# Kernel optimization log

Measured on AMD Instinct MI355X. Metric: run time of the kernel, lower is better.

The kernel has to match this reference:

```python
import jax, jax.numpy as jnp
import numpy as np

N, E, C, H0, H1 = 100_000, 1_600_000, 32, 128, 64


def _sage(x, src, dst, wl, bl, wr, n):
    # PyG SAGEConv(aggr='min'): lin_l(min_{j in N(i)} x_j) + lin_r(x_i); lin_r has no bias.
    agg = jax.ops.segment_min(x[src], dst, num_segments=n)  # [n, d]
    # nodes with no in-edges: PyG fills with 0 (segment_min yields dtype max)
    agg = jnp.where(agg >= jnp.finfo(x.dtype).max, jnp.zeros((), x.dtype), agg)
    return agg @ wl + bl + x @ wr


def _bn(x, g, b, eps=1e-5):
    # training-mode BatchNorm over the node dimension
    mu = jnp.mean(x, axis=0)
    var = jnp.var(x, axis=0)
    return (x - mu) * jax.lax.rsqrt(var + eps) * g + b


def _forward(x, edge_index,
             rm1_wl, rm1_bl, rm1_wr, rmn1_g, rmn1_b,
             rm2_wl, rm2_bl, rm2_wr, rmn2_g, rmn2_b,
             rm4_wl, rm4_bl, rm4_wr,
             sh1_wl, sh1_bl, sh1_wr, shn1_g, shn1_b,
             rt1_wl, rt1_bl, rt1_wr, rtn1_g, rtn1_b, rt3_w, rt3_b,
             md1_wl, md1_bl, md1_wr, mdn1_g, mdn1_b, md3_w, md3_b):
    n = x.shape[0]
    src, dst = edge_index[0], edge_index[1]
    rm = jax.nn.relu(_bn(_sage(x, src, dst, rm1_wl, rm1_bl, rm1_wr, n), rmn1_g, rmn1_b))
    rm = jax.nn.relu(_bn(_sage(rm, src, dst, rm2_wl, rm2_bl, rm2_wr, n), rmn2_g, rmn2_b))
    rm = _sage(rm, src, dst, rm4_wl, rm4_bl, rm4_wr, n)  # [n, 3]
    xs = jnp.concatenate([x, rm], axis=1)  # [n, C+3]
    xs = jax.nn.relu(_bn(_sage(xs, src, dst, sh1_wl, sh1_bl, sh1_wr, n), shn1_g, shn1_b))
    rm_ls = jax.nn.log_softmax(rm, axis=1)
    labels = (jnp.argmax(rm_ls, axis=1) == 2).astype(x.dtype)  # [n]
    rt = jax.nn.relu(_bn(_sage(xs, src, dst, rt1_wl, rt1_bl, rt1_wr, n), rtn1_g, rtn1_b))
    rt = (rt @ rt3_w + rt3_b).ravel() * labels
    md = jax.nn.relu(_bn(_sage(xs, src, dst, md1_wl, md1_bl, md1_wr, n), mdn1_g, mdn1_b))
    md = (md @ md3_w + md3_b).ravel() * labels
    return rm_ls, rt, md


def setup_inputs() -> dict:
    key = jax.random.key(0)
    ks = iter(jax.random.split(key, 64))

    def w(shape):
        s = 1.0 / np.sqrt(shape[0])
        return jax.random.uniform(next(ks), shape, jnp.float32, -s, s)

    inp = {
        "x": jax.random.normal(next(ks), (N, C), jnp.float32),
        "edge_index": jax.random.randint(next(ks), (2, E), 0, N, dtype=jnp.int32),
    }

    def sage_params(cin, cout, name):
        inp[name + "_wl"] = w((cin, cout))
        inp[name + "_bl"] = jnp.zeros((cout,), jnp.float32)
        inp[name + "_wr"] = w((cin, cout))

    def bn_params(c, name):
        inp[name + "_g"] = jnp.ones((c,), jnp.float32)
        inp[name + "_b"] = jnp.zeros((c,), jnp.float32)

    sage_params(C, H0, "rm1"); bn_params(H0, "rmn1")
    sage_params(H0, H1, "rm2"); bn_params(H1, "rmn2")
    sage_params(H1, 3, "rm4")
    sage_params(C + 3, H0, "sh1"); bn_params(H0, "shn1")
    sage_params(H0, H1, "rt1"); bn_params(H1, "rtn1")
    inp["rt3_w"] = w((H1, 1)); inp["rt3_b"] = jnp.zeros((1,), jnp.float32)
    sage_params(H0, H1, "md1"); bn_params(H1, "mdn1")
    inp["md3_w"] = w((H1, 1)); inp["md3_b"] = jnp.zeros((1,), jnp.float32)
    return inp


def reference(x, edge_index,
              rm1_wl, rm1_bl, rm1_wr, rmn1_g, rmn1_b,
              rm2_wl, rm2_bl, rm2_wr, rmn2_g, rmn2_b,
              rm4_wl, rm4_bl, rm4_wr,
              sh1_wl, sh1_bl, sh1_wr, shn1_g, shn1_b,
              rt1_wl, rt1_bl, rt1_wr, rtn1_g, rtn1_b, rt3_w, rt3_b,
              md1_wl, md1_bl, md1_wr, mdn1_g, mdn1_b, md3_w, md3_b):
    return _forward(x, edge_index,
                    rm1_wl, rm1_bl, rm1_wr, rmn1_g, rmn1_b,
                    rm2_wl, rm2_bl, rm2_wr, rmn2_g, rmn2_b,
                    rm4_wl, rm4_bl, rm4_wr,
                    sh1_wl, sh1_bl, sh1_wr, shn1_g, shn1_b,
                    rt1_wl, rt1_bl, rt1_wr, rtn1_g, rtn1_b, rt3_w, rt3_b,
                    md1_wl, md1_bl, md1_wr, mdn1_g, mdn1_b, md3_w, md3_b)
```

## Files before the change

kernel.cpp:

```cpp
#include <hip/hip_runtime.h>

#define FLTMAX 3.402823466e+38f
#define DEV __device__ __forceinline__

typedef unsigned short u16;
typedef unsigned int u32;
typedef __bf16 bf16_t;
typedef bf16_t bf16x8 __attribute__((ext_vector_type(8)));
typedef float f32x4 __attribute__((ext_vector_type(4)));

union U16x8 { uint4 u; bf16x8 b; };

DEV float trf(float v, float a, float b) { return fmaxf(fmaf(v, a, b), 0.f); }

DEV float sfmin(float m, float v, u32 sm) {
    return fminf(m, __uint_as_float(__float_as_uint(v) ^ sm));
}
DEV float sdec(float m, u32 sm) { return __uint_as_float(__float_as_uint(m) ^ sm); }

DEV u16 f2bf(float f) {
    u32 u = __float_as_uint(f);
    return (u16)((u + 0x7FFFu + ((u >> 16) & 1u)) >> 16);
}

__global__ __launch_bounds__(256) void hist_k(const int* __restrict__ dst,
                                              int* __restrict__ deg, int E) {
    int e = blockIdx.x * 256 + threadIdx.x;
    if (e >= E) return;
    atomicAdd(&deg[dst[e]], 1);
}

__global__ __launch_bounds__(256) void scan_block_k(const int* __restrict__ deg,
                                                    int* __restrict__ ptr,
                                                    int* __restrict__ bsum, int n) {
    __shared__ int ls[256];
    int i = blockIdx.x * 256 + threadIdx.x;
    int v = (i < n) ? deg[i] : 0;
    ls[threadIdx.x] = v;
    __syncthreads();
#pragma unroll
    for (int off = 1; off < 256; off <<= 1) {
        int a = (threadIdx.x >= off) ? ls[threadIdx.x - off] : 0;
        __syncthreads();
        ls[threadIdx.x] += a;
        __syncthreads();
    }
    if (i < n) ptr[i] = ls[threadIdx.x] - v;
    if (threadIdx.x == 255) bsum[blockIdx.x] = ls[255];
}

__global__ __launch_bounds__(512) void scan_bsum_k(int* __restrict__ bsum, int nb) {
    __shared__ int ls[512];
    int t = threadIdx.x;
    int v = (t < nb) ? bsum[t] : 0;
    ls[t] = v;
    __syncthreads();
#pragma unroll
    for (int off = 1; off < 512; off <<= 1) {
        int a = (t >= off) ? ls[t - off] : 0;
        __syncthreads();
        ls[t] += a;
        __syncthreads();
    }
    if (t < nb) bsum[t] = ls[t] - v;
}

__global__ __launch_bounds__(256) void scan_add_k(int* __restrict__ ptr,
                                                  int* __restrict__ pos,
                                                  const int* __restrict__ bsum,
                                                  int n, int E) {
    int i = blockIdx.x * 256 + threadIdx.x;
    if (i == 0) ptr[n] = E;
    if (i < n) {
        int p = ptr[i] + bsum[blockIdx.x];
        ptr[i] = p;
        pos[i] = p;
    }
}

__global__ __launch_bounds__(256) void csr_fill_part_k(
    const int* __restrict__ src, const int* __restrict__ dst,
    int* __restrict__ pos, int* __restrict__ csr, int E, int lo_step) {
    const int part = blockIdx.x & 7;
    const int e = (blockIdx.x >> 3) * 256 + threadIdx.x;
    if (e >= E) return;
    const int d = dst[e];
    const int lo = part * lo_step;
    const int hi = lo + lo_step;
    if (d < lo || d >= hi) return;
    const int p = atomicAdd(&pos[d], 1);
    csr[p] = src[e];
}

__global__ __launch_bounds__(256) void gather_min32_k(
    const float* __restrict__ feat, const int* __restrict__ ptr,
    const int* __restrict__ csr, float* __restrict__ agg, int n) {
    const int lane = threadIdx.x & 63;
    const int wave = (blockIdx.x * 256 + threadIdx.x) >> 6;
    const int node = wave * 2 + (lane >> 5);
    if (node >= n) return;
    const int fl = lane & 31;
    int e = ptr[node];
    const int end = ptr[node + 1];
    const bool empty = (e == end);
    float m = FLTMAX;
    for (; e + 7 < end; e += 8) {
        int s[8];
#pragma unroll
        for (int j = 0; j < 8; j++) s[j] = csr[e + j];
        float v[8];
#pragma unroll
        for (int j = 0; j < 8; j++) v[j] = feat[(size_t)s[j] * 32 + fl];
#pragma unroll
        for (int j = 0; j < 8; j++) m = fminf(m, v[j]);
    }
    for (; e < end; e++) m = fminf(m, feat[(size_t)csr[e] * 32 + fl]);
    agg[(size_t)node * 32 + fl] = empty ? 0.f : m;
}

__global__ __launch_bounds__(256) void gather_min128_k(
    const float* __restrict__ feat, const int* __restrict__ ptr,
    const int* __restrict__ csr, const float* __restrict__ coef,
    float* __restrict__ agg, int n) {
    const int lane = threadIdx.x & 63;
    const int wave = (blockIdx.x * 256 + threadIdx.x) >> 6;
    const int node = wave * 2 + (lane >> 5);
    if (node >= n) return;
    const int fl = (lane & 31) * 4;
    const float4 ca = *(const float4*)(coef + fl);
    const float4 cb = *(const float4*)(coef + 128 + fl);
    const u32 sm0 = (ca.x < 0.f) ? 0x80000000u : 0u;
    const u32 sm1 = (ca.y < 0.f) ? 0x80000000u : 0u;
    const u32 sm2 = (ca.z < 0.f) ? 0x80000000u : 0u;
    const u32 sm3 = (ca.w < 0.f) ? 0x80000000u : 0u;
    int e = ptr[node];
    const int end = ptr[node + 1];
    const bool empty = (e == end);
    float m0 = FLTMAX, m1 = FLTMAX, m2 = FLTMAX, m3 = FLTMAX;
    for (; e + 7 < end; e += 8) {
        int s[8];
#pragma unroll
        for (int j = 0; j < 8; j++) s[j] = csr[e + j];
        float4 v[8];
#pragma unroll
        for (int j = 0; j < 8; j++) v[j] = *(const float4*)(feat + (size_t)s[j] * 128 + fl);
#pragma unroll
        for (int j = 0; j < 8; j++) {
            m0 = sfmin(m0, v[j].x, sm0);
            m1 = sfmin(m1, v[j].y, sm1);
            m2 = sfmin(m2, v[j].z, sm2);
            m3 = sfmin(m3, v[j].w, sm3);
        }
    }
    for (; e + 3 < end; e += 4) {
        int s[4];
#pragma unroll
        for (int j = 0; j < 4; j++) s[j] = csr[e + j];
        float4 v[4];
#pragma unroll
        for (int j = 0; j < 4; j++) v[j] = *(const float4*)(feat + (size_t)s[j] * 128 + fl);
#pragma unroll
        for (int j = 0; j < 4; j++) {
            m0 = sfmin(m0, v[j].x, sm0);
            m1 = sfmin(m1, v[j].y, sm1);
            m2 = sfmin(m2, v[j].z, sm2);
            m3 = sfmin(m3, v[j].w, sm3);
        }
    }
    for (; e < end; e++) {
        const float4 v = *(const float4*)(feat + (size_t)csr[e] * 128 + fl);
        m0 = sfmin(m0, v.x, sm0);
        m1 = sfmin(m1, v.y, sm1);
        m2 = sfmin(m2, v.z, sm2);
        m3 = sfmin(m3, v.w, sm3);
    }
    float4 o;
    o.x = empty ? 0.f : trf(sdec(m0, sm0), ca.x, cb.x);
    o.y = empty ? 0.f : trf(sdec(m1, sm1), ca.y, cb.y);
    o.z = empty ? 0.f : trf(sdec(m2, sm2), ca.z, cb.z);
    o.w = empty ? 0.f : trf(sdec(m3, sm3), ca.w, cb.w);
    *(float4*)(agg + (size_t)node * 128 + fl) = o;
}

__global__ __launch_bounds__(256) void gather_bf_k(
    u16* __restrict__ Acat, const int* __restrict__ ptr,
    const int* __restrict__ csr, int n) {
    const int lane = threadIdx.x & 63;
    const int wave = (blockIdx.x * 256 + threadIdx.x) >> 6;
    const int node = wave * 2 + (lane >> 5);
    if (node >= n) return;
    const int fl = (lane & 31) * 4;
    int e = ptr[node];
    const int end = ptr[node + 1];
    uint2 outv = {0u, 0u};
    if (e != end) {
        float m0 = FLTMAX, m1 = FLTMAX, m2 = FLTMAX, m3 = FLTMAX;
        for (; e + 7 < end; e += 8) {
            int s[8];
#pragma unroll
            for (int j = 0; j < 8; j++) s[j] = csr[e + j];
            uint2 v[8];
#pragma unroll
            for (int j = 0; j < 8; j++) v[j] = *(const uint2*)(Acat + (size_t)s[j] * 256 + 128 + fl);
#pragma unroll
            for (int j = 0; j < 8; j++) {
                m0 = fminf(m0, __uint_as_float(v[j].x << 16));
                m1 = fminf(m1, __uint_as_float(v[j].x & 0xffff0000u));
                m2 = fminf(m2, __uint_as_float(v[j].y << 16));
                m3 = fminf(m3, __uint_as_float(v[j].y & 0xffff0000u));
            }
        }
        for (; e < end; e++) {
            const uint2 v = *(const uint2*)(Acat + (size_t)csr[e] * 256 + 128 + fl);
            m0 = fminf(m0, __uint_as_float(v.x << 16));
            m1 = fminf(m1, __uint_as_float(v.x & 0xffff0000u));
            m2 = fminf(m2, __uint_as_float(v.y << 16));
            m3 = fminf(m3, __uint_as_float(v.y & 0xffff0000u));
        }
        outv.x = (__float_as_uint(m0) >> 16) | (__float_as_uint(m1) & 0xffff0000u);
        outv.y = (__float_as_uint(m2) >> 16) | (__float_as_uint(m3) & 0xffff0000u);
    }
    *(uint2*)(Acat + (size_t)node * 256 + fl) = outv;
}

__global__ __launch_bounds__(256) void gather_min3_k(
    const float* __restrict__ feat, const int* __restrict__ ptr,
    const int* __restrict__ csr, float* __restrict__ agg, int n) {
    int i = blockIdx.x * 256 + threadIdx.x;
    if (i >= n) return;
    int e = ptr[i], end = ptr[i + 1];
    bool empty = (e == end);
    float m0 = FLTMAX, m1 = FLTMAX, m2 = FLTMAX;
    for (; e < end; e++) {
        const float* r = feat + (size_t)csr[e] * 3;
        m0 = fminf(m0, r[0]);
        m1 = fminf(m1, r[1]);
        m2 = fminf(m2, r[2]);
    }
    agg[(size_t)i * 3 + 0] = empty ? 0.f : m0;
    agg[(size_t)i * 3 + 1] = empty ? 0.f : m1;
    agg[(size_t)i * 3 + 2] = empty ? 0.f : m2;
}

__global__ __launch_bounds__(256) void convert_k(
    const float* __restrict__ h, const float* __restrict__ coef,
    u16* __restrict__ Acat, int n) {
    int t = blockIdx.x * 256 + threadIdx.x;
    int total = n * 32;
    if (t >= total) return;
    int i = t >> 5;
    int dq = (t & 31) * 4;
    const float4 hv = *(const float4*)(h + (size_t)i * 128 + dq);
    const float4 ca = *(const float4*)(coef + dq);
    const float4 cb = *(const float4*)(coef + 128 + dq);
    ushort4 o;
    o.x = f2bf(trf(hv.x, ca.x, cb.x));
    o.y = f2bf(trf(hv.y, ca.y, cb.y));
    o.z = f2bf(trf(hv.z, ca.z, cb.z));
    o.w = f2bf(trf(hv.w, ca.w, cb.w));
    *(ushort4*)(Acat + (size_t)i * 256 + 128 + dq) = o;
}

__global__ __launch_bounds__(256) void wprep_dual_k(
    const float* __restrict__ rwl, const float* __restrict__ rwr,
    const float* __restrict__ mwl, const float* __restrict__ mwr,
    u16* __restrict__ WT) {
    int t = blockIdx.x * 256 + threadIdx.x;
    int c = t >> 8;
    int k = t & 255;
    const float* wlp = (c < 64) ? rwl : mwl;
    const float* wrp = (c < 64) ? rwr : mwr;
    const int cc = c & 63;
    float v = (k < 128) ? wlp[k * 64 + cc] : wrp[(k - 128) * 64 + cc];
    WT[(size_t)c * 256 + k] = f2bf(v);
}

__global__ __launch_bounds__(256) void gemm_bf_k(
    const u16* __restrict__ A, const u16* __restrict__ WT,
    const float* __restrict__ bl1, const float* __restrict__ bl2,
    float* __restrict__ out, float* __restrict__ bpart, int n) {
    constexpr int NT = 8;
    __shared__ float bs[256];
    const int tid = threadIdx.x;
    bs[tid] = 0.f;
    const int wave = tid >> 6, lane = tid & 63;
    const int quad = lane >> 4, l16 = lane & 15;
    const int row0 = blockIdx.x * 64 + wave * 16;
    const int rowA = min(row0 + l16, n - 1);
    const uint4* Arow = (const uint4*)(A + (size_t)rowA * 256) + quad;

    bf16x8 a[8];
#pragma unroll
    for (int kc = 0; kc < 8; kc++) {
        U16x8 u; u.u = Arow[kc * 4];
        a[kc] = u.b;
    }
    f32x4 acc[NT];
#pragma unroll
    for (int i = 0; i < NT; i++) acc[i] = (f32x4){0.f, 0.f, 0.f, 0.f};
#pragma unroll
    for (int nt = 0; nt < NT; nt++) {
        const uint4* Brow = (const uint4*)(WT + (size_t)(nt * 16 + l16) * 256) + quad;
#pragma unroll
        for (int kc = 0; kc < 8; kc++) {
            U16x8 u; u.u = Brow[kc * 4];
            acc[nt] = __builtin_amdgcn_mfma_f32_16x16x32_bf16(a[kc], u.b, acc[nt], 0, 0, 0);
        }
    }
    __syncthreads();
#pragma unroll
    for (int nt = 0; nt < NT; nt++) {
        const int col = nt * 16 + l16;
        const float bias = (col < 64) ? bl1[col] : bl2[col - 64];
        float s = 0.f, q = 0.f;
#pragma unroll
        for (int r = 0; r < 4; r++) {
            const int row = row0 + quad * 4 + r;
            if (row < n) {
                const float o = acc[nt][r] + bias;
                out[(size_t)row * 128 + col] = o;
                s += o;
                q += o * o;
            }
        }
        atomicAdd(&bs[col], s);
        atomicAdd(&bs[128 + col], q);
    }
    __syncthreads();
    bpart[(size_t)blockIdx.x * 256 + tid] = bs[tid];
}

__global__ __launch_bounds__(256) void linear1s_k(
    const float* __restrict__ agg, const float* __restrict__ h,
    const float* __restrict__ wl, const float* __restrict__ bl,
    const float* __restrict__ wr, float* __restrict__ out,
    float* __restrict__ bpart, int n) {
    constexpr int DOUT = 128, CT = 32, RB = 32, LDW = 36;
    __shared__ float Ash[RB * LDW];
    __shared__ float Hsh[RB * LDW];
    const int tid = threadIdx.x;
    const int base = blockIdx.x * RB;
    {
        const int sr = tid >> 3;
        const int col = (tid & 7) * 4;
        const int grow = min(base + sr, n - 1);
        *(float4*)(Ash + sr * LDW + col) = *(const float4*)(agg + (size_t)grow * 32 + col);
        *(float4*)(Hsh + sr * LDW + col) = *(const float4*)(h + (size_t)grow * 32 + col);
    }
    __syncthreads();
    const int ct = tid % CT;
    const int rt = tid / CT;
    const int col = ct * 4;
    const int row0 = base + rt * 4;
    float4 acc[4] = {};
#pragma unroll 2
    for (int k0 = 0; k0 < 32; k0 += 4) {
        float4 wlv[4], wrv[4];
#pragma unroll
        for (int j = 0; j < 4; j++) {
            wlv[j] = *(const float4*)(wl + (size_t)(k0 + j) * DOUT + col);
            wrv[j] = *(const float4*)(wr + (size_t)(k0 + j) * DOUT + col);
        }
#pragma unroll
        for (int r = 0; r < 4; r++) {
            const float4 av = *(const float4*)(Ash + (rt * 4 + r) * LDW + k0);
            const float4 hv = *(const float4*)(Hsh + (rt * 4 + r) * LDW + k0);
#pragma unroll
            for (int j = 0; j < 4; j++) {
                const float aa = j == 0 ? av.x : j == 1 ? av.y : j == 2 ? av.z : av.w;
                const float bb = j == 0 ? hv.x : j == 1 ? hv.y : j == 2 ? hv.z : hv.w;
                acc[r].x += aa * wlv[j].x + bb * wrv[j].x;
                acc[r].y += aa * wlv[j].y + bb * wrv[j].y;
                acc[r].z += aa * wlv[j].z + bb * wrv[j].z;
                acc[r].w += aa * wlv[j].w + bb * wrv[j].w;
            }
        }
    }
    const float4 bv = *(const float4*)(bl + col);
    float cs[4] = {}, cq[4] = {};
#pragma unroll
    for (int r = 0; r < 4; r++) {
        if (row0 + r < n) {
            float4 o = acc[r];
            o.x += bv.x; o.y += bv.y; o.z += bv.z; o.w += bv.w;
            *(float4*)(out + (size_t)(row0 + r) * DOUT + col) = o;
            cs[0] += o.x; cq[0] += o.x * o.x;
            cs[1] += o.y; cq[1] += o.y * o.y;
            cs[2] += o.z; cq[2] += o.z * o.z;
            cs[3] += o.w; cq[3] += o.w * o.w;
        }
    }
    __syncthreads();
#pragma unroll
    for (int j = 0; j < 4; j++) Ash[tid * 4 + j] = cs[j];
    __syncthreads();
    if (tid < CT) {
#pragma unroll
        for (int j = 0; j < 4; j++) {
            float s = 0.f;
#pragma unroll
            for (int k = 0; k < 8; k++) s += Ash[(tid + k * CT) * 4 + j];
            bpart[(size_t)blockIdx.x * 256 + tid * 4 + j] = s;
        }
    }
    __syncthreads();
#pragma unroll
    for (int j = 0; j < 4; j++) Ash[tid * 4 + j] = cq[j];
    __syncthreads();
    if (tid < CT) {
#pragma unroll
        for (int j = 0; j < 4; j++) {
            float s = 0.f;
#pragma unroll
            for (int k = 0; k < 8; k++) s += Ash[(tid + k * CT) * 4 + j];
            bpart[(size_t)blockIdx.x * 256 + 128 + tid * 4 + j] = s;
        }
    }
}

__global__ __launch_bounds__(256) void linear2_k(
    const float* __restrict__ agg, const float* __restrict__ h,
    const float* __restrict__ coef, const float* __restrict__ wl,
    const float* __restrict__ bl, const float* __restrict__ wr,
    float* __restrict__ out, float* __restrict__ bpart, int n) {
    constexpr int DIN = 128, DOUT = 64, CT = 16, RB = 64, LDW = 132;
    __shared__ float Ash[RB * LDW];
    __shared__ float Hsh[RB * LDW];
    const int tid = threadIdx.x;
    const int base = blockIdx.x * RB;
    {
        const int sr = tid >> 2;
        const int sc = tid & 3;
        const int grow = min(base + sr, n - 1);
        const float* ar = agg + (size_t)grow * DIN;
        const float* hr = h + (size_t)grow * DIN;
#pragma unroll
        for (int c = 0; c < 8; c++) {
            const int col = (sc + c * 4) * 4;
            const float4 av = *(const float4*)(ar + col);
            float4 hv = *(const float4*)(hr + col);
            const float4 ca = *(const float4*)(coef + col);
            const float4 cb = *(const float4*)(coef + DIN + col);
            hv.x = trf(hv.x, ca.x, cb.x); hv.y = trf(hv.y, ca.y, cb.y);
            hv.z = trf(hv.z, ca.z, cb.z); hv.w = trf(hv.w, ca.w, cb.w);
            *(float4*)(Ash + sr * LDW + col) = av;
            *(float4*)(Hsh + sr * LDW + col) = hv;
        }
    }
    __syncthreads();
    const int ct = tid % CT;
    const int rt = tid / CT;
    const int col = ct * 4;
    const int row0 = base + rt * 4;
    float4 acc[4] = {};
#pragma unroll 2
    for (int k0 = 0; k0 < DIN; k0 += 4) {
        float4 wlv[4], wrv[4];
#pragma unroll
        for (int j = 0; j < 4; j++) {
            wlv[j] = *(const float4*)(wl + (size_t)(k0 + j) * DOUT + col);
            wrv[j] = *(const float4*)(wr + (size_t)(k0 + j) * DOUT + col);
        }
#pragma unroll
        for (int r = 0; r < 4; r++) {
            const float4 av = *(const float4*)(Ash + (rt * 4 + r) * LDW + k0);
            const float4 hv = *(const float4*)(Hsh + (rt * 4 + r) * LDW + k0);
#pragma unroll
            for (int j = 0; j < 4; j++) {
                const float aa = j == 0 ? av.x : j == 1 ? av.y : j == 2 ? av.z : av.w;
                const float bb = j == 0 ? hv.x : j == 1 ? hv.y : j == 2 ? hv.z : hv.w;
                acc[r].x += aa * wlv[j].x + bb * wrv[j].x;
                acc[r].y += aa * wlv[j].y + bb * wrv[j].y;
                acc[r].z += aa * wlv[j].z + bb * wrv[j].z;
                acc[r].w += aa * wlv[j].w + bb * wrv[j].w;
            }
        }
    }
    const float4 bv = *(const float4*)(bl + col);
    float cs[4] = {}, cq[4] = {};
#pragma unroll
    for (int r = 0; r < 4; r++) {
        if (row0 + r < n) {
            float4 o = acc[r];
            o.x += bv.x; o.y += bv.y; o.z += bv.z; o.w += bv.w;
            *(float4*)(out + (size_t)(row0 + r) * DOUT + col) = o;
            cs[0] += o.x; cq[0] += o.x * o.x;
            cs[1] += o.y; cq[1] += o.y * o.y;
            cs[2] += o.z; cq[2] += o.z * o.z;
            cs[3] += o.w; cq[3] += o.w * o.w;
        }
    }
    __syncthreads();
#pragma unroll
    for (int j = 0; j < 4; j++) Ash[tid * 4 + j] = cs[j];
    __syncthreads();
    if (tid < CT) {
#pragma unroll
        for (int j = 0; j < 4; j++) {
            float s = 0.f;
#pragma unroll
            for (int k = 0; k < 16; k++) s += Ash[(tid + k * CT) * 4 + j];
            bpart[(size_t)blockIdx.x * 128 + tid * 4 + j] = s;
        }
    }
    __syncthreads();
#pragma unroll
    for (int j = 0; j < 4; j++) Ash[tid * 4 + j] = cq[j];
    __syncthreads();
    if (tid < CT) {
#pragma unroll
        for (int j = 0; j < 4; j++) {
            float s = 0.f;
#pragma unroll
            for (int k = 0; k < 16; k++) s += Ash[(tid + k * CT) * 4 + j];
            bpart[(size_t)blockIdx.x * 128 + 64 + tid * 4 + j] = s;
        }
    }
}

__global__ __launch_bounds__(256) void linear_shs_k(
    const float* __restrict__ aggx, const float* __restrict__ x,
    const float* __restrict__ aggr, const float* __restrict__ rm,
    const float* __restrict__ wl, const float* __restrict__ bl,
    const float* __restrict__ wr, float* __restrict__ out,
    float* __restrict__ bpart, int n) {
    constexpr int DOUT = 128, CT = 32, RB = 32, LDW = 36;
    __shared__ float Ash[RB * LDW];
    __shared__ float Hsh[RB * LDW];
    __shared__ float Rsh[RB * 4], Msh[RB * 4];
    const int tid = threadIdx.x;
    const int base = blockIdx.x * RB;
    {
        const int sr = tid >> 3;
        const int col = (tid & 7) * 4;
        const int grow = min(base + sr, n - 1);
        *(float4*)(Ash + sr * LDW + col) = *(const float4*)(aggx + (size_t)grow * 32 + col);
        *(float4*)(Hsh + sr * LDW + col) = *(const float4*)(x + (size_t)grow * 32 + col);
        if (tid < RB) {
            const int gr = min(base + tid, n - 1);
#pragma unroll
            for (int k = 0; k < 3; k++) {
                Rsh[tid * 4 + k] = aggr[(size_t)gr * 3 + k];
                Msh[tid * 4 + k] = rm[(size_t)gr * 3 + k];
            }
        }
    }
    __syncthreads();
    const int ct = tid % CT;
    const int rt = tid / CT;
    const int col = ct * 4;
    const int row0 = base + rt * 4;
    float4 acc[4] = {};
#pragma unroll 2
    for (int k0 = 0; k0 < 32; k0 += 4) {
        float4 wlv[4], wrv[4];
#pragma unroll
        for (int j = 0; j < 4; j++) {
            wlv[j] = *(const float4*)(wl + (size_t)(k0 + j) * DOUT + col);
            wrv[j] = *(const float4*)(wr + (size_t)(k0 + j) * DOUT + col);
        }
#pragma unroll
        for (int r = 0; r < 4; r++) {
            const float4 av = *(const float4*)(Ash + (rt * 4 + r) * LDW + k0);
            const float4 hv = *(const float4*)(Hsh + (rt * 4 + r) * LDW + k0);
#pragma unroll
            for (int j = 0; j < 4; j++) {
                const float aa = j == 0 ? av.x : j == 1 ? av.y : j == 2 ? av.z : av.w;
                const float bb = j == 0 ? hv.x : j == 1 ? hv.y : j == 2 ? hv.z : hv.w;
                acc[r].x += aa * wlv[j].x + bb * wrv[j].x;
                acc[r].y += aa * wlv[j].y + bb * wrv[j].y;
                acc[r].z += aa * wlv[j].z + bb * wrv[j].z;
                acc[r].w += aa * wlv[j].w + bb * wrv[j].w;
            }
        }
    }
#pragma unroll
    for (int k = 0; k < 3; k++) {
        const float4 wlv = *(const float4*)(wl + (size_t)(32 + k) * DOUT + col);
        const float4 wrv = *(const float4*)(wr + (size_t)(32 + k) * DOUT + col);
#pragma unroll
        for (int r = 0; r < 4; r++) {
            const float a = Rsh[(rt * 4 + r) * 4 + k];
            const float b = Msh[(rt * 4 + r) * 4 + k];
            acc[r].x += a * wlv.x + b * wrv.x;
            acc[r].y += a * wlv.y + b * wrv.y;
            acc[r].z += a * wlv.z + b * wrv.z;
            acc[r].w += a * wlv.w + b * wrv.w;
        }
    }
    const float4 bv = *(const float4*)(bl + col);
    float cs[4] = {}, cq[4] = {};
#pragma unroll
    for (int r = 0; r < 4; r++) {
        if (row0 + r < n) {
            float4 o = acc[r];
            o.x += bv.x; o.y += bv.y; o.z += bv.z; o.w += bv.w;
            *(float4*)(out + (size_t)(row0 + r) * DOUT + col) = o;
            cs[0] += o.x; cq[0] += o.x * o.x;
            cs[1] += o.y; cq[1] += o.y * o.y;
            cs[2] += o.z; cq[2] += o.z * o.z;
            cs[3] += o.w; cq[3] += o.w * o.w;
        }
    }
    __syncthreads();
#pragma unroll
    for (int j = 0; j < 4; j++) Ash[tid * 4 + j] = cs[j];
    __syncthreads();
    if (tid < CT) {
#pragma unroll
        for (int j = 0; j < 4; j++) {
            float s = 0.f;
#pragma unroll
            for (int k = 0; k < 8; k++) s += Ash[(tid + k * CT) * 4 + j];
            bpart[(size_t)blockIdx.x * 256 + tid * 4 + j] = s;
        }
    }
    __syncthreads();
#pragma unroll
    for (int j = 0; j < 4; j++) Ash[tid * 4 + j] = cq[j];
    __syncthreads();
    if (tid < CT) {
#pragma unroll
        for (int j = 0; j < 4; j++) {
            float s = 0.f;
#pragma unroll
            for (int k = 0; k < 8; k++) s += Ash[(tid + k * CT) * 4 + j];
            bpart[(size_t)blockIdx.x * 256 + 128 + tid * 4 + j] = s;
        }
    }
}

__global__ __launch_bounds__(256) void reduce_part_k(
    const float* __restrict__ bpart, float* __restrict__ stats,
    int nb, int width) {
    const int c = threadIdx.x;
    if (c >= width) return;
    float s = 0.f;
    for (int k = blockIdx.x; k < nb; k += gridDim.x)
        s += bpart[(size_t)k * width + c];
    atomicAdd(&stats[c], s);
}

template <int D>
__global__ void coef_k(const float* __restrict__ stats, const float* __restrict__ g,
                       const float* __restrict__ bb, float* __restrict__ coef,
                       float invN) {
    int d = threadIdx.x;
    if (d >= D) return;
    float mu = stats[d] * invN;
    float var = stats[D + d] * invN - mu * mu;
    float a = rsqrtf(var + 1e-5f) * g[d];
    coef[d] = a;
    coef[D + d] = bb[d] - mu * a;
}

__global__ void coef_dual_k(const float* __restrict__ stats,
                            const float* __restrict__ gR, const float* __restrict__ bR,
                            const float* __restrict__ gM, const float* __restrict__ bM,
                            float* __restrict__ coefR, float* __restrict__ coefM,
                            float invN) {
    int d = threadIdx.x;
    if (d >= 128) return;
    float mu = stats[d] * invN;
    float var = stats[128 + d] * invN - mu * mu;
    bool isR = d < 64;
    int c = isR ? d : d - 64;
    float g = isR ? gR[c] : gM[c];
    float be = isR ? bR[c] : bM[c];
    float a = rsqrtf(var + 1e-5f) * g;
    float* co = isR ? coefR : coefM;
    co[c] = a;
    co[64 + c] = be - mu * a;
}

__global__ __launch_bounds__(256) void rm_fused_k(
    const float* __restrict__ h2, const float* __restrict__ coef,
    const int* __restrict__ ptr, const int* __restrict__ csr,
    const float* __restrict__ wl, const float* __restrict__ bl,
    const float* __restrict__ wr, float* __restrict__ rmb,
    float* __restrict__ ls_out, float* __restrict__ lab, int n) {
    const int lane = threadIdx.x & 63;
    const int node = (blockIdx.x * 256 + threadIdx.x) >> 6;
    if (node >= n) return;
    const float a = coef[lane], b = coef[64 + lane];
    const u32 sm = (a < 0.f) ? 0x80000000u : 0u;
    int e = ptr[node];
    const int end = ptr[node + 1];
    const bool empty = (e == end);
    float m = FLTMAX;
    for (; e + 15 < end; e += 16) {
        int s[16];
#pragma unroll
        for (int j = 0; j < 16; j++) s[j] = csr[e + j];
        float v[16];
#pragma unroll
        for (int j = 0; j < 16; j++) v[j] = h2[(size_t)s[j] * 64 + lane];
#pragma unroll
        for (int j = 0; j < 16; j++) m = sfmin(m, v[j], sm);
    }
    for (; e + 3 < end; e += 4) {
        int s[4];
#pragma unroll
        for (int j = 0; j < 4; j++) s[j] = csr[e + j];
        float v[4];
#pragma unroll
        for (int j = 0; j < 4; j++) v[j] = h2[(size_t)s[j] * 64 + lane];
#pragma unroll
        for (int j = 0; j < 4; j++) m = sfmin(m, v[j], sm);
    }
    for (; e < end; e++) m = sfmin(m, h2[(size_t)csr[e] * 64 + lane], sm);
    const float mv = empty ? 0.f : trf(sdec(m, sm), a, b);
    const float hv = trf(h2[(size_t)node * 64 + lane], a, b);
    float c0 = mv * wl[lane * 3 + 0] + hv * wr[lane * 3 + 0];
    float c1 = mv * wl[lane * 3 + 1] + hv * wr[lane * 3 + 1];
    float c2 = mv * wl[lane * 3 + 2] + hv * wr[lane * 3 + 2];
#pragma unroll
    for (int off = 1; off < 64; off <<= 1) {
        c0 += __shfl_xor(c0, off);
        c1 += __shfl_xor(c1, off);
        c2 += __shfl_xor(c2, off);
    }
    const float r0 = c0 + bl[0], r1 = c1 + bl[1], r2 = c2 + bl[2];
    if (lane < 3) {
        const float r = lane == 0 ? r0 : lane == 1 ? r1 : r2;
        rmb[(size_t)node * 3 + lane] = r;
        const float mx = fmaxf(r0, fmaxf(r1, r2));
        const float lse = mx + logf(expf(r0 - mx) + expf(r1 - mx) + expf(r2 - mx));
        ls_out[(size_t)node * 3 + lane] = r - lse;
        if (lane == 0) lab[node] = (r2 > r0 && r2 > r1) ? 1.f : 0.f;
    }
}

__global__ __launch_bounds__(256) void final_k(
    const float* __restrict__ rtmd,
    const float* __restrict__ cR, const float* __restrict__ cM,
    const float* __restrict__ rtw, const float* __restrict__ rtb,
    const float* __restrict__ mdw, const float* __restrict__ mdb,
    const float* __restrict__ lab, float* __restrict__ out_rt,
    float* __restrict__ out_md, int n) {
    const int lane = threadIdx.x & 63;
    const int node = (blockIdx.x * 256 + threadIdx.x) >> 6;
    if (node >= n) return;
    const float* rr = rtmd + (size_t)node * 128;
    float a = trf(rr[lane], cR[lane], cR[64 + lane]) * rtw[lane];
    float b = trf(rr[64 + lane], cM[lane], cM[64 + lane]) * mdw[lane];
#pragma unroll
    for (int off = 1; off < 64; off <<= 1) {
        a += __shfl_xor(a, off);
        b += __shfl_xor(b, off);
    }
    if (lane == 0) {
        const float l = lab[node];
        out_rt[node] = (a + rtb[0]) * l;
        out_md[node] = (b + mdb[0]) * l;
    }
}

extern "C" void kernel_launch(void* const* d_in, const int* in_sizes, int n_in,
                              void* d_out, int out_size, void* d_ws, size_t ws_size,
                              hipStream_t stream) {
    const float* x = (const float*)d_in[0];
    const int* ei = (const int*)d_in[1];
    const int E = in_sizes[1] / 2;
    const int n = in_sizes[0] / 32;
    const int* src = ei;
    const int* dst = ei + E;

    const float* rm1_wl = (const float*)d_in[2];
    const float* rm1_bl = (const float*)d_in[3];
    const float* rm1_wr = (const float*)d_in[4];
    const float* rmn1_g = (const float*)d_in[5];
    const float* rmn1_b = (const float*)d_in[6];
    const float* rm2_wl = (const float*)d_in[7];
    const float* rm2_bl = (const float*)d_in[8];
    const float* rm2_wr = (const float*)d_in[9];
    const float* rmn2_g = (const float*)d_in[10];
    const float* rmn2_b = (const float*)d_in[11];
    const float* rm4_wl = (const float*)d_in[12];
    const float* rm4_bl = (const float*)d_in[13];
    const float* rm4_wr = (const float*)d_in[14];
    const float* sh1_wl = (const float*)d_in[15];
    const float* sh1_bl = (const float*)d_in[16];
    const float* sh1_wr = (const float*)d_in[17];
    const float* shn1_g = (const float*)d_in[18];
    const float* shn1_b = (const float*)d_in[19];
    const float* rt1_wl = (const float*)d_in[20];
    const float* rt1_bl = (const float*)d_in[21];
    const float* rt1_wr = (const float*)d_in[22];
    const float* rtn1_g = (const float*)d_in[23];
    const float* rtn1_b = (const float*)d_in[24];
    const float* rt3_w = (const float*)d_in[25];
    const float* rt3_b = (const float*)d_in[26];
    const float* md1_wl = (const float*)d_in[27];
    const float* md1_bl = (const float*)d_in[28];
    const float* md1_wr = (const float*)d_in[29];
    const float* mdn1_g = (const float*)d_in[30];
    const float* mdn1_b = (const float*)d_in[31];
    const float* md3_w = (const float*)d_in[32];
    const float* md3_b = (const float*)d_in[33];

    char* w = (char*)d_ws;
    float* aggX  = (float*)w; w += (size_t)n * 32 * 4;
    float* h1    = (float*)w; w += (size_t)n * 128 * 4;
    char*  shbuf = w;         w += (size_t)n * 512;
    float* h2rt  = (float*)w; w += (size_t)n * 128 * 4;
    float* rmb   = (float*)w; w += (size_t)n * 3 * 4;
    float* aggR  = (float*)w; w += (size_t)n * 3 * 4;
    float* lab   = (float*)w; w += (size_t)n * 4;
    float* stats = (float*)w; w += 1024 * 4;
    float* coef  = (float*)w; w += 1024 * 4;
    u16*   WTD   = (u16*)w;   w += (size_t)128 * 256 * 2;
    int* ptr  = (int*)w; w += (size_t)(n + 1) * 4;
    int* pos  = (int*)w; w += (size_t)n * 4;
    int* bsum = (int*)w; w += 1024 * 4;
    int* csr  = (int*)w; w += (size_t)E * 4;

    float* aggB = (float*)shbuf;
    u16*   Acat = (u16*)shbuf;
    float* h2 = h2rt;
    float* rtmd = h2rt;
    float* stats1 = stats, *stats2 = stats + 256, *statsSh = stats + 512, *statsD = stats + 768;
    float* coef1 = coef, *coef2 = coef + 256, *coefSh = coef + 384;
    float* coefRt = coef + 640, *coefMd = coef + 768;

    float* bp1  = (float*)shbuf;
    float* bp2  = rmb;
    float* bpSh = (float*)shbuf;
    float* bpD  = rmb;

    float* out = (float*)d_out;
    float* out_ls = out;
    float* out_rt = out + (size_t)3 * n;
    float* out_md = out + (size_t)4 * n;

    const float invN = 1.f / (float)n;
    auto cdiv = [](int a, int b) { return (a + b - 1) / b; };
    const int nb = cdiv(n, 256);
    const int nb32 = cdiv(n, 32);
    const int nb64 = cdiv(n, 64);

    hipMemsetAsync(stats, 0, 1024 * 4, stream);
    hipMemsetAsync(pos, 0, (size_t)n * 4, stream);

    hist_k<<<cdiv(E, 256), 256, 0, stream>>>(dst, pos, E);
    wprep_dual_k<<<128, 256, 0, stream>>>(rt1_wl, rt1_wr, md1_wl, md1_wr, WTD);
    scan_block_k<<<nb, 256, 0, stream>>>(pos, ptr, bsum, n);
    scan_bsum_k<<<1, 512, 0, stream>>>(bsum, nb);
    scan_add_k<<<nb, 256, 0, stream>>>(ptr, pos, bsum, n, E);
    csr_fill_part_k<<<cdiv(E, 256) * 8, 256, 0, stream>>>(src, dst, pos, csr, E, cdiv(n, 8));

    gather_min32_k<<<cdiv(n, 8), 256, 0, stream>>>(x, ptr, csr, aggX, n);
    linear1s_k<<<nb32, 256, 0, stream>>>(aggX, x, rm1_wl, rm1_bl, rm1_wr, h1, bp1, n);
    reduce_part_k<<<64, 256, 0, stream>>>(bp1, stats1, nb32, 256);
    coef_k<128><<<1, 128, 0, stream>>>(stats1, rmn1_g, rmn1_b, coef1, invN);

    gather_min128_k<<<cdiv(n, 8), 256, 0, stream>>>(h1, ptr, csr, coef1, aggB, n);
    linear2_k<<<nb64, 256, 0, stream>>>(aggB, h1, coef1, rm2_wl, rm2_bl, rm2_wr, h2, bp2, n);
    reduce_part_k<<<64, 256, 0, stream>>>(bp2, stats2, nb64, 128);
    coef_k<64><<<1, 64, 0, stream>>>(stats2, rmn2_g, rmn2_b, coef2, invN);

    rm_fused_k<<<cdiv(n, 4), 256, 0, stream>>>(h2, coef2, ptr, csr, rm4_wl, rm4_bl, rm4_wr, rmb, out_ls, lab, n);

    gather_min3_k<<<cdiv(n, 256), 256, 0, stream>>>(rmb, ptr, csr, aggR, n);
    linear_shs_k<<<nb32, 256, 0, stream>>>(aggX, x, aggR, rmb, sh1_wl, sh1_bl, sh1_wr, h1, bpSh, n);
    reduce_part_k<<<64, 256, 0, stream>>>(bpSh, statsSh, nb32, 256);
    coef_k<128><<<1, 128, 0, stream>>>(statsSh, shn1_g, shn1_b, coefSh, invN);

    convert_k<<<cdiv(n * 32, 256), 256, 0, stream>>>(h1, coefSh, Acat, n);
    gather_bf_k<<<cdiv(n, 8), 256, 0, stream>>>(Acat, ptr, csr, n);
    gemm_bf_k<<<nb64, 256, 0, stream>>>(Acat, WTD, rt1_bl, md1_bl, rtmd, bpD, n);
    reduce_part_k<<<64, 256, 0, stream>>>(bpD, statsD, nb64, 256);
    coef_dual_k<<<1, 128, 0, stream>>>(statsD, rtn1_g, rtn1_b, mdn1_g, mdn1_b, coefRt, coefMd, invN);

    final_k<<<cdiv(n, 4), 256, 0, stream>>>(rtmd, coefRt, coefMd,
                                            rt3_w, rt3_b, md3_w, md3_b, lab,
                                            out_rt, out_md, n);
}
```

Measured before the change: 872.4 us.

## Fold BN coef computation, bsum scan and min3 gather into consumer kernels

Removes the standalone coef_k/coef_dual_k launches by having each consumer kernel compute BatchNorm scale and shift from the raw stats. The single-block bsum scan is folded into scan_add_k, where each block sums its prefix of block totals. The 3-wide min gather is moved into linear_shs_k, with 8 lanes per row and a shuffle reduction. gather_min128 now uses one wave per node with float2 loads instead of half-wave float4. This cuts about six small serial launches, at the cost of redundant per-thread coefficient math and a change in gather access width.

```diff
diff --git a/kernel.cpp b/kernel.cpp
--- a/kernel.cpp
+++ b/kernel.cpp
@@ -21,6 +21,13 @@
 DEV u16 f2bf(float f) {
     u32 u = __float_as_uint(f);
     return (u16)((u + 0x7FFFu + ((u >> 16) & 1u)) >> 16);
+}
+
+DEV void bncoef(float s, float s2, float g, float be, float invN, float& a, float& b) {
+    const float mu = s * invN;
+    const float var = s2 * invN - mu * mu;
+    a = rsqrtf(var + 1e-5f) * g;
+    b = be - mu * a;
 }
 
 __global__ __launch_bounds__(256) void hist_k(const int* __restrict__ dst,
@@ -49,30 +56,23 @@
     if (threadIdx.x == 255) bsum[blockIdx.x] = ls[255];
 }
 
-__global__ __launch_bounds__(512) void scan_bsum_k(int* __restrict__ bsum, int nb) {
-    __shared__ int ls[512];
-    int t = threadIdx.x;
-    int v = (t < nb) ? bsum[t] : 0;
-    ls[t] = v;
-    __syncthreads();
-#pragma unroll
-    for (int off = 1; off < 512; off <<= 1) {
-        int a = (t >= off) ? ls[t - off] : 0;
-        __syncthreads();
-        ls[t] += a;
-        __syncthreads();
-    }
-    if (t < nb) bsum[t] = ls[t] - v;
-}
-
 __global__ __launch_bounds__(256) void scan_add_k(int* __restrict__ ptr,
                                                   int* __restrict__ pos,
                                                   const int* __restrict__ bsum,
                                                   int n, int E) {
-    int i = blockIdx.x * 256 + threadIdx.x;
+    __shared__ int shw[4];
+    const int tid = threadIdx.x;
+    int part = 0;
+    for (int k = tid; k < blockIdx.x; k += 256) part += bsum[k];
+#pragma unroll
+    for (int off = 1; off < 64; off <<= 1) part += __shfl_xor(part, off);
+    if ((tid & 63) == 0) shw[tid >> 6] = part;
+    __syncthreads();
+    const int boff = shw[0] + shw[1] + shw[2] + shw[3];
+    const int i = blockIdx.x * 256 + tid;
     if (i == 0) ptr[n] = E;
     if (i < n) {
-        int p = ptr[i] + bsum[blockIdx.x];
+        int p = ptr[i] + boff;
         ptr[i] = p;
         pos[i] = p;
     }
@@ -120,66 +120,61 @@
 
 __global__ __launch_bounds__(256) void gather_min128_k(
     const float* __restrict__ feat, const int* __restrict__ ptr,
-    const int* __restrict__ csr, const float* __restrict__ coef,
-    float* __restrict__ agg, int n) {
+    const int* __restrict__ csr, const float* __restrict__ stats,
+    const float* __restrict__ g, const float* __restrict__ be,
+    float* __restrict__ coef_out, float* __restrict__ agg, float invN, int n) {
     const int lane = threadIdx.x & 63;
-    const int wave = (blockIdx.x * 256 + threadIdx.x) >> 6;
-    const int node = wave * 2 + (lane >> 5);
+    const int node = (blockIdx.x * 256 + threadIdx.x) >> 6;
     if (node >= n) return;
-    const int fl = (lane & 31) * 4;
-    const float4 ca = *(const float4*)(coef + fl);
-    const float4 cb = *(const float4*)(coef + 128 + fl);
-    const u32 sm0 = (ca.x < 0.f) ? 0x80000000u : 0u;
-    const u32 sm1 = (ca.y < 0.f) ? 0x80000000u : 0u;
-    const u32 sm2 = (ca.z < 0.f) ? 0x80000000u : 0u;
-    const u32 sm3 = (ca.w < 0.f) ? 0x80000000u : 0u;
+    const int fl = lane * 2;
+    float ca0, cb0, ca1, cb1;
+    bncoef(stats[fl], stats[128 + fl], g[fl], be[fl], invN, ca0, cb0);
+    bncoef(stats[fl + 1], stats[129 + fl], g[fl + 1], be[fl + 1], invN, ca1, cb1);
+    if (blockIdx.x == 0 && threadIdx.x < 64) {
+        coef_out[fl] = ca0; coef_out[fl + 1] = ca1;
+        coef_out[128 + fl] = cb0; coef_out[129 + fl] = cb1;
+    }
+    const u32 sm0 = (ca0 < 0.f) ? 0x80000000u : 0u;
+    const u32 sm1 = (ca1 < 0.f) ? 0x80000000u : 0u;
     int e = ptr[node];
     const int end = ptr[node + 1];
     const bool empty = (e == end);
-    float m0 = FLTMAX, m1 = FLTMAX, m2 = FLTMAX, m3 = FLTMAX;
+    float m0 = FLTMAX, m1 = FLTMAX;
     for (; e + 7 < end; e += 8) {
         int s[8];
 #pragma unroll
         for (int j = 0; j < 8; j++) s[j] = csr[e + j];
-        float4 v[8];
-#pragma unroll
-        for (int j = 0; j < 8; j++) v[j] = *(const float4*)(feat + (size_t)s[j] * 128 + fl);
+        float2 v[8];
+#pragma unroll
+        for (int j = 0; j < 8; j++) v[j] = *(const float2*)(feat + (size_t)s[j] * 128 + fl);
 #pragma unroll
         for (int j = 0; j < 8; j++) {
             m0 = sfmin(m0, v[j].x, sm0);
             m1 = sfmin(m1, v[j].y, sm1);
-            m2 = sfmin(m2, v[j].z, sm2);
-            m3 = sfmin(m3, v[j].w, sm3);
         }
     }
     for (; e + 3 < end; e += 4) {
         int s[4];
 #pragma unroll
         for (int j = 0; j < 4; j++) s[j] = csr[e + j];
-        float4 v[4];
-#pragma unroll
-        for (int j = 0; j < 4; j++) v[j] = *(const float4*)(feat + (size_t)s[j] * 128 + fl);
+        float2 v[4];
+#pragma unroll
+        for (int j = 0; j < 4; j++) v[j] = *(const float2*)(feat + (size_t)s[j] * 128 + fl);
 #pragma unroll
         for (int j = 0; j < 4; j++) {
             m0 = sfmin(m0, v[j].x, sm0);
             m1 = sfmin(m1, v[j].y, sm1);
-            m2 = sfmin(m2, v[j].z, sm2);
-            m3 = sfmin(m3, v[j].w, sm3);
         }
     }
     for (; e < end; e++) {
-        const float4 v = *(const float4*)(feat + (size_t)csr[e] * 128 + fl);
+        const float2 v = *(const float2*)(feat + (size_t)csr[e] * 128 + fl);
         m0 = sfmin(m0, v.x, sm0);
         m1 = sfmin(m1, v.y, sm1);
-        m2 = sfmin(m2, v.z, sm2);
-        m3 = sfmin(m3, v.w, sm3);
-    }
-    float4 o;
-    o.x = empty ? 0.f : trf(sdec(m0, sm0), ca.x, cb.x);
-    o.y = empty ? 0.f : trf(sdec(m1, sm1), ca.y, cb.y);
-    o.z = empty ? 0.f : trf(sdec(m2, sm2), ca.z, cb.z);
-    o.w = empty ? 0.f : trf(sdec(m3, sm3), ca.w, cb.w);
-    *(float4*)(agg + (size_t)node * 128 + fl) = o;
+    }
+    float2 o;
+    o.x = empty ? 0.f : trf(sdec(m0, sm0), ca0, cb0);
+    o.y = empty ? 0.f : trf(sdec(m1, sm1), ca1, cb1);
+    *(float2*)(agg + (size_t)node * 128 + fl) = o;
 }
 
 __global__ __launch_bounds__(256) void gather_bf_k(
@@ -223,36 +218,25 @@
     *(uint2*)(Acat + (size_t)node * 256 + fl) = outv;
 }
 
-__global__ __launch_bounds__(256) void gather_min3_k(
-    const float* __restrict__ feat, const int* __restrict__ ptr,
-    const int* __restrict__ csr, float* __restrict__ agg, int n) {
-    int i = blockIdx.x * 256 + threadIdx.x;
-    if (i >= n) return;
-    int e = ptr[i], end = ptr[i + 1];
-    bool empty = (e == end);
-    float m0 = FLTMAX, m1 = FLTMAX, m2 = FLTMAX;
-    for (; e < end; e++) {
-        const float* r = feat + (size_t)csr[e] * 3;
-        m0 = fminf(m0, r[0]);
-        m1 = fminf(m1, r[1]);
-        m2 = fminf(m2, r[2]);
-    }
-    agg[(size_t)i * 3 + 0] = empty ? 0.f : m0;
-    agg[(size_t)i * 3 + 1] = empty ? 0.f : m1;
-    agg[(size_t)i * 3 + 2] = empty ? 0.f : m2;
-}
-
 __global__ __launch_bounds__(256) void convert_k(
-    const float* __restrict__ h, const float* __restrict__ coef,
-    u16* __restrict__ Acat, int n) {
+    const float* __restrict__ h, const float* __restrict__ stats,
+    const float* __restrict__ g, const float* __restrict__ be,
+    u16* __restrict__ Acat, float invN, int n) {
     int t = blockIdx.x * 256 + threadIdx.x;
     int total = n * 32;
     if (t >= total) return;
     int i = t >> 5;
     int dq = (t & 31) * 4;
+    const float4 s1 = *(const float4*)(stats + dq);
+    const float4 s2 = *(const float4*)(stats + 128 + dq);
+    const float4 gv = *(const float4*)(g + dq);
+    const float4 ev = *(const float4*)(be + dq);
+    float4 ca, cb;
+    bncoef(s1.x, s2.x, gv.x, ev.x, invN, ca.x, cb.x);
+    bncoef(s1.y, s2.y, gv.y, ev.y, invN, ca.y, cb.y);
+    bncoef(s1.z, s2.z, gv.z, ev.z, invN, ca.z, cb.z);
+    bncoef(s1.w, s2.w, gv.w, ev.w, invN, ca.w, cb.w);
     const float4 hv = *(const float4*)(h + (size_t)i * 128 + dq);
-    const float4 ca = *(const float4*)(coef + dq);
-    const float4 cb = *(const float4*)(coef + 128 + dq);
     ushort4 o;
     o.x = f2bf(trf(hv.x, ca.x, cb.x));
     o.y = f2bf(trf(hv.y, ca.y, cb.y));
@@ -520,7 +504,8 @@
 
 __global__ __launch_bounds__(256) void linear_shs_k(
     const float* __restrict__ aggx, const float* __restrict__ x,
-    const float* __restrict__ aggr, const float* __restrict__ rm,
+    const float* __restrict__ rmb, const int* __restrict__ ptr,
+    const int* __restrict__ csr,
     const float* __restrict__ wl, const float* __restrict__ bl,
     const float* __restrict__ wr, float* __restrict__ out,
     float* __restrict__ bpart, int n) {
@@ -536,13 +521,30 @@
         const int grow = min(base + sr, n - 1);
         *(float4*)(Ash + sr * LDW + col) = *(const float4*)(aggx + (size_t)grow * 32 + col);
         *(float4*)(Hsh + sr * LDW + col) = *(const float4*)(x + (size_t)grow * 32 + col);
-        if (tid < RB) {
-            const int gr = min(base + tid, n - 1);
-#pragma unroll
-            for (int k = 0; k < 3; k++) {
-                Rsh[tid * 4 + k] = aggr[(size_t)gr * 3 + k];
-                Msh[tid * 4 + k] = rm[(size_t)gr * 3 + k];
-            }
+        const int sub = tid & 7;
+        const int e0 = ptr[grow];
+        const int end2 = ptr[grow + 1];
+        float q0 = FLTMAX, q1 = FLTMAX, q2 = FLTMAX;
+        for (int e = e0 + sub; e < end2; e += 8) {
+            const float* rr = rmb + (size_t)csr[e] * 3;
+            q0 = fminf(q0, rr[0]);
+            q1 = fminf(q1, rr[1]);
+            q2 = fminf(q2, rr[2]);
+        }
+#pragma unroll
+        for (int off = 1; off < 8; off <<= 1) {
+            q0 = fminf(q0, __shfl_xor(q0, off));
+            q1 = fminf(q1, __shfl_xor(q1, off));
+            q2 = fminf(q2, __shfl_xor(q2, off));
+        }
+        if (sub == 0) {
+            const bool em = (e0 == end2);
+            Rsh[sr * 4 + 0] = em ? 0.f : q0;
+            Rsh[sr * 4 + 1] = em ? 0.f : q1;
+            Rsh[sr * 4 + 2] = em ? 0.f : q2;
+            Msh[sr * 4 + 0] = rmb[(size_t)grow * 3 + 0];
+            Msh[sr * 4 + 1] = rmb[(size_t)grow * 3 + 1];
+            Msh[sr * 4 + 2] = rmb[(size_t)grow * 3 + 2];
         }
     }
     __syncthreads();
@@ -641,48 +643,18 @@
     atomicAdd(&stats[c], s);
 }
 
-template <int D>
-__global__ void coef_k(const float* __restrict__ stats, const float* __restrict__ g,
-                       const float* __restrict__ bb, float* __restrict__ coef,
-                       float invN) {
-    int d = threadIdx.x;
-    if (d >= D) return;
-    float mu = stats[d] * invN;
-    float var = stats[D + d] * invN - mu * mu;
-    float a = rsqrtf(var + 1e-5f) * g[d];
-    coef[d] = a;
-    coef[D + d] = bb[d] - mu * a;
-}
-
-__global__ void coef_dual_k(const float* __restrict__ stats,
-                            const float* __restrict__ gR, const float* __restrict__ bR,
-                            const float* __restrict__ gM, const float* __restrict__ bM,
-                            float* __restrict__ coefR, float* __restrict__ coefM,
-                            float invN) {
-    int d = threadIdx.x;
-    if (d >= 128) return;
-    float mu = stats[d] * invN;
-    float var = stats[128 + d] * invN - mu * mu;
-    bool isR = d < 64;
-    int c = isR ? d : d - 64;
-    float g = isR ? gR[c] : gM[c];
-    float be = isR ? bR[c] : bM[c];
-    float a = rsqrtf(var + 1e-5f) * g;
-    float* co = isR ? coefR : coefM;
-    co[c] = a;
-    co[64 + c] = be - mu * a;
-}
-
 __global__ __launch_bounds__(256) void rm_fused_k(
-    const float* __restrict__ h2, const float* __restrict__ coef,
+    const float* __restrict__ h2, const float* __restrict__ stats,
+    const float* __restrict__ g, const float* __restrict__ be,
     const int* __restrict__ ptr, const int* __restrict__ csr,
     const float* __restrict__ wl, const float* __restrict__ bl,
     const float* __restrict__ wr, float* __restrict__ rmb,
-    float* __restrict__ ls_out, float* __restrict__ lab, int n) {
+    float* __restrict__ ls_out, float* __restrict__ lab, float invN, int n) {
     const int lane = threadIdx.x & 63;
     const int node = (blockIdx.x * 256 + threadIdx.x) >> 6;
     if (node >= n) return;
-    const float a = coef[lane], b = coef[64 + lane];
+    float a, b;
+    bncoef(stats[lane], stats[64 + lane], g[lane], be[lane], invN, a, b);
     const u32 sm = (a < 0.f) ? 0x80000000u : 0u;
     int e = ptr[node];
     const int end = ptr[node + 1];
@@ -732,18 +704,22 @@
 }
 
 __global__ __launch_bounds__(256) void final_k(
-    const float* __restrict__ rtmd,
-    const float* __restrict__ cR, const float* __restrict__ cM,
+    const float* __restrict__ rtmd, const float* __restrict__ stats,
+    const float* __restrict__ gR, const float* __restrict__ bR,
+    const float* __restrict__ gM, const float* __restrict__ bM,
     const float* __restrict__ rtw, const float* __restrict__ rtb,
     const float* __restrict__ mdw, const float* __restrict__ mdb,
     const float* __restrict__ lab, float* __restrict__ out_rt,
-    float* __restrict__ out_md, int n) {
+    float* __restrict__ out_md, float invN, int n) {
     const int lane = threadIdx.x & 63;
     const int node = (blockIdx.x * 256 + threadIdx.x) >> 6;
     if (node >= n) return;
+    float aR, bRc, aM, bMc;
+    bncoef(stats[lane], stats[128 + lane], gR[lane], bR[lane], invN, aR, bRc);
+    bncoef(stats[64 + lane], stats[192 + lane], gM[lane], bM[lane], invN, aM, bMc);
     const float* rr = rtmd + (size_t)node * 128;
-    float a = trf(rr[lane], cR[lane], cR[64 + lane]) * rtw[lane];
-    float b = trf(rr[64 + lane], cM[lane], cM[64 + lane]) * mdw[lane];
+    float a = trf(rr[lane], aR, bRc) * rtw[lane];
+    float b = trf(rr[64 + lane], aM, bMc) * mdw[lane];
 #pragma unroll
     for (int off = 1; off < 64; off <<= 1) {
         a += __shfl_xor(a, off);
@@ -820,8 +796,7 @@
     float* h2 = h2rt;
     float* rtmd = h2rt;
     float* stats1 = stats, *stats2 = stats + 256, *statsSh = stats + 512, *statsD = stats + 768;
-    float* coef1 = coef, *coef2 = coef + 256, *coefSh = coef + 384;
-    float* coefRt = coef + 640, *coefMd = coef + 768;
+    float* coef1 = coef;
 
     float* bp1  = (float*)shbuf;
     float* bp2  = rmb;
@@ -845,34 +820,31 @@
     hist_k<<<cdiv(E, 256), 256, 0, stream>>>(dst, pos, E);
     wprep_dual_k<<<128, 256, 0, stream>>>(rt1_wl, rt1_wr, md1_wl, md1_wr, WTD);
     scan_block_k<<<nb, 256, 0, stream>>>(pos, ptr, bsum, n);
-    scan_bsum_k<<<1, 512, 0, stream>>>(bsum, nb);
     scan_add_k<<<nb, 256, 0, stream>>>(ptr, pos, bsum, n, E);
     csr_fill_part_k<<<cdiv(E, 256) * 8, 256, 0, stream>>>(src, dst, pos, csr, E, cdiv(n, 8));
 
     gather_min32_k<<<cdiv(n, 8), 256, 0, stream>>>(x, ptr, csr, aggX, n);
     linear1s_k<<<nb32, 256, 0, stream>>>(aggX, x, rm1_wl, rm1_bl, rm1_wr, h1, bp1, n);
     reduce_part_k<<<64, 256, 0, stream>>>(bp1, stats1, nb32, 256);
-    coef_k<128><<<1, 128, 0, stream>>>(stats1, rmn1_g, rmn1_b, coef1, invN);
-
-    gather_min128_k<<<cdiv(n, 8), 256, 0, stream>>>(h1, ptr, csr, coef1, aggB, n);
+
+    gather_min128_k<<<cdiv(n, 4), 256, 0, stream>>>(h1, ptr, csr, stats1, rmn1_g, rmn1_b,
+                                                    coef1, aggB, invN, n);
     linear2_k<<<nb64, 256, 0, stream>>>(aggB, h1, coef1, rm2_wl, rm2_bl, rm2_wr, h2, bp2, n);
     reduce_part_k<<<64, 256, 0, stream>>>(bp2, stats2, nb64, 128);
-    coef_k<64><<<1, 64, 0, stream>>>(stats2, rmn2_g, rmn2_b, coef2, invN);
-
-    rm_fused_k<<<cdiv(n, 4), 256, 0, stream>>>(h2, coef2, ptr, csr, rm4_wl, rm4_bl, rm4_wr, rmb, out_ls, lab, n);
-
-    gather_min3_k<<<cdiv(n, 256), 256, 0, stream>>>(rmb, ptr, csr, aggR, n);
-    linear_shs_k<<<nb32, 256, 0, stream>>>(aggX, x, aggR, rmb, sh1_wl, sh1_bl, sh1_wr, h1, bpSh, n);
+
+    rm_fused_k<<<cdiv(n, 4), 256, 0, stream>>>(h2, stats2, rmn2_g, rmn2_b, ptr, csr,
+                                               rm4_wl, rm4_bl, rm4_wr, rmb, out_ls, lab, invN, n);
+
+    linear_shs_k<<<nb32, 256, 0, stream>>>(aggX, x, rmb, ptr, csr,
+                                           sh1_wl, sh1_bl, sh1_wr, h1, bpSh, n);
     reduce_part_k<<<64, 256, 0, stream>>>(bpSh, statsSh, nb32, 256);
-    coef_k<128><<<1, 128, 0, stream>>>(statsSh, shn1_g, shn1_b, coefSh, invN);
-
-    convert_k<<<cdiv(n * 32, 256), 256, 0, stream>>>(h1, coefSh, Acat, n);
+
+    convert_k<<<cdiv(n * 32, 256), 256, 0, stream>>>(h1, statsSh, shn1_g, shn1_b, Acat, invN, n);
     gather_bf_k<<<cdiv(n, 8), 256, 0, stream>>>(Acat, ptr, csr, n);
     gemm_bf_k<<<nb64, 256, 0, stream>>>(Acat, WTD, rt1_bl, md1_bl, rtmd, bpD, n);
     reduce_part_k<<<64, 256, 0, stream>>>(bpD, statsD, nb64, 256);
-    coef_dual_k<<<1, 128, 0, stream>>>(statsD, rtn1_g, rtn1_b, mdn1_g, mdn1_b, coefRt, coefMd, invN);
-
-    final_k<<<cdiv(n, 4), 256, 0, stream>>>(rtmd, coefRt, coefMd,
+
+    final_k<<<cdiv(n, 4), 256, 0, stream>>>(rtmd, statsD, rtn1_g, rtn1_b, mdn1_g, mdn1_b,
                                             rt3_w, rt3_b, md3_w, md3_b, lab,
-                                            out_rt, out_md, n);
-}
+                                            out_rt, out_md, invN, n);
+}
```

Measured after the change: 850.9 us. 2.5% less time.
